# Kernel tuning notes

Measured on AMD Instinct MI355X. Metric: run time of the kernel, lower is better.

The kernel has to match this reference:

```python
import jax, jax.numpy as jnp
import numpy as np
from jax import lax

KH = KW = 3
STRIDE = (1, 1)
PAD = (1, 1)

def setup_inputs() -> dict:
    key = jax.random.key(0)
    k1, k2, k3 = jax.random.split(key, 3)
    B_, C, H, W = 16, 128, 56, 56
    O, R = 256, 16
    Kflat = C * KH * KW
    x = jax.random.normal(k1, (B_, C, H, W), dtype=jnp.float32)
    # kaiming_normal_ fan_out for A: std = sqrt(2/out_channels)
    A = jax.random.normal(k2, (O, R), dtype=jnp.float32) * np.float32(np.sqrt(2.0 / O))
    # kaiming_normal_ fan_in for B: std = sqrt(2/kernel_flat_dim)
    Bm = jax.random.normal(k3, (R, Kflat), dtype=jnp.float32) * np.float32(np.sqrt(2.0 / Kflat))
    return {"x": x, "A": A, "B": Bm}

def reference(x, A, B):
    b, c, h, w = x.shape
    h_out = (h + 2 * PAD[0] - KH) // STRIDE[0] + 1
    w_out = (w + 2 * PAD[1] - KW) // STRIDE[1] + 1
    # im2col: [B, C*KH*KW, H_out, W_out]; feature order (c, kh, kw) matches torch Unfold
    patches = lax.conv_general_dilated_patches(
        x, filter_shape=(KH, KW), window_strides=STRIDE,
        padding=((PAD[0], PAD[0]), (PAD[1], PAD[1])))
    patches = patches.reshape(b, c * KH * KW, h_out * w_out)  # [B, K, L]
    tmp = jnp.einsum('rk,bkl->brl', B, patches)               # rank-limited matmul
    out = jnp.einsum('or,brl->bol', A, tmp)                   # [B, O, L]
    return out.reshape(b, A.shape[0], h_out, w_out)
```

## Files before the change

kernel.cpp:

```cpp
#include <hip/hip_runtime.h>
#include <hip/hip_bf16.h>


#define Bn 16
#define Cc 128
#define Hh 56
#define Ww 56
#define Ll (Hh * Ww)
#define Rr 16
#define Oo 256
#define KF (Cc * 9)
#define NKS 36
#define W2 58
#define RPITCH 128
#define ROWB (W2 * RPITCH)
#define HB 2

typedef __attribute__((ext_vector_type(8))) short bfrag_t;
typedef __attribute__((ext_vector_type(4))) float f32x4;

__device__ __forceinline__ float bf16_bits(unsigned short u) {
    return __uint_as_float(((unsigned)u) << 16);
}

__device__ __forceinline__ unsigned short bf16_rne(float f) {
    const unsigned u = __float_as_uint(f);
    const unsigned r = u + 0x7FFFu + ((u >> 16) & 1u);
    return (unsigned short)(r >> 16);
}

__device__ __forceinline__ bool detect_bf16(const void* __restrict__ p) {
    const unsigned* w = (const unsigned*)p;
    int c = 0;
#pragma unroll
    for (int i = 0; i < 32; ++i) {
        const unsigned e = (w[i] >> 7) & 0xFFu;
        c += (e >= 96u && e <= 144u) ? 1 : 0;
    }
    return c >= 20;
}

__global__ __launch_bounds__(256) void prep_frag(
    const void* __restrict__ A, const void* __restrict__ Bm,
    unsigned short* __restrict__ Bfrag, float* __restrict__ Afp)
{
    const bool ab = detect_bf16(A);
    const bool bb = detect_bf16(Bm);
    const int i = blockIdx.x * 256 + threadIdx.x;
    if (i < NKS * 512) {
        const int kstep = i >> 9, rem = i & 511;
        const int l = rem >> 3, e = rem & 7;
        const int r = l & 15, g = l >> 4;
        const int kp = kstep * 32 + g * 8 + e;
        const int tap = kp >> 7, c = kp & 127;
        const int k = c * 9 + tap;
        const float v = bb ? bf16_bits(((const unsigned short*)Bm)[r * KF + k])
                           : ((const float*)Bm)[r * KF + k];
        const unsigned short hi = bf16_rne(v);
        const float lov = v - bf16_bits(hi);
        Bfrag[(kstep * 2 + 0) * 512 + rem] = hi;
        Bfrag[(kstep * 2 + 1) * 512 + rem] = bf16_rne(lov);
    }
    if (i < Oo * Rr) {
        Afp[i] = ab ? bf16_bits(((const unsigned short*)A)[i])
                    : ((const float*)A)[i];
    }
}

#define MFB(A, B, C) __builtin_amdgcn_mfma_f32_16x16x32_bf16((A), (B), (C), 0, 0, 0)

template<bool XB, bool BB>
__device__ __forceinline__ void fused_body(
    const void* __restrict__ x,
    const unsigned short* __restrict__ Bfrag,
    const float* __restrict__ Afp,
    float* __restrict__ out,
    unsigned short* __restrict__ xs)
{
    const int tid  = threadIdx.x;
    const int lane = tid & 63;
    const int wv   = __builtin_amdgcn_readfirstlane(tid >> 6);
    const int t    = wv & 3;
    const int kh   = wv >> 2;
    const int h0   = blockIdx.x * HB;
    const int b    = blockIdx.y;

    {
        const int l   = lane;
        const bool lok = (l < Ww);
#pragma unroll
        for (int rr = 0; rr < HB + 2; ++rr) {
            const int hh = h0 - 1 + rr;
            unsigned short* xr = xs + rr * ROWB;
            if (hh >= 0 && hh < Hh) {
                if (lok) {
                    const unsigned gb = (unsigned)(b * Cc * Ll + hh * Ww + l);
#pragma unroll
                    for (int it = 0; it < 2; ++it) {
                        const int cs_ = it * 8 + wv;
                        const int c0  = cs_ * 8;
                        bfrag_t v;
#pragma unroll
                        for (int j = 0; j < 8; ++j) {
                            if constexpr (XB) {
                                v[j] = (short)((const unsigned short*)x)[
                                    gb + (unsigned)((c0 + j) * Ll)];
                            } else {
                                v[j] = (short)bf16_rne(((const float*)x)[
                                    gb + (unsigned)((c0 + j) * Ll)]);
                            }
                        }
                        const int sp = cs_ ^ ((l + 1) & 7);
                        *(bfrag_t*)((char*)xr + (l + 1) * 256 + sp * 16) = v;
                    }
                }
            } else {
                unsigned* xw = (unsigned*)xr;
#pragma unroll
                for (int it = 0; it < 7; ++it) xw[it * 512 + tid] = 0u;
                if (tid < 3712 - 7 * 512) xw[7 * 512 + tid] = 0u;
            }
        }
        if (tid < 128) {
#pragma unroll
            for (int rr = 0; rr < HB + 2; ++rr) {
                xs[rr * ROWB + tid] = 0;
                xs[rr * ROWB + 57 * RPITCH + tid] = 0;
            }
        }
    }
    __syncthreads();

    const int col = lane & 15;
    const int g   = lane >> 4;
    const int px  = t * 16 + col;
    const int pxc = px < Ww ? px : Ww - 1;

    unsigned off6[6];
#pragma unroll
    for (int dwv = 0; dwv < 3; ++dwv)
#pragma unroll
        for (int cbi = 0; cbi < 2; ++cbi) {
            const int cb = kh * 2 + cbi;
            const int p2 = pxc + dwv;
            off6[dwv * 2 + cbi] = (unsigned)(p2 * 256 +
                (((cb * 4 + g) ^ (p2 & 7)) << 4));
        }

    f32x4 acc0 = {0.f, 0.f, 0.f, 0.f};
    f32x4 acc1 = {0.f, 0.f, 0.f, 0.f};
    const bfrag_t* __restrict__ bfp = (const bfrag_t*)Bfrag;

#pragma unroll
    for (int tap = 0; tap < 9; ++tap) {
        const int dh = tap / 3, dw = tap - dh * 3;
#pragma unroll
        for (int cbi = 0; cbi < 2; ++cbi) {
            const int cb = kh * 2 + cbi;
            const int ks = tap * 4 + cb;
            const bfrag_t ahi = bfp[(ks * 2 + 0) * 64 + lane];
            const char* p0 = (const char*)xs + dh * (ROWB * 2) + off6[dw * 2 + cbi];
            const bfrag_t pf0 = *(const bfrag_t*)p0;
            const bfrag_t pf1 = *(const bfrag_t*)(p0 + ROWB * 2);
            acc0 = MFB(ahi, pf0, acc0);
            acc1 = MFB(ahi, pf1, acc1);
            if constexpr (!BB) {
                const bfrag_t alo = bfp[(ks * 2 + 1) * 64 + lane];
                acc0 = MFB(alo, pf0, acc0);
                acc1 = MFB(alo, pf1, acc1);
            }
        }
    }

    __syncthreads();
    float (*tmp2)[HB][Rr][66] = (float (*)[HB][Rr][66])xs;

#pragma unroll
    for (int reg = 0; reg < 4; ++reg) {
        tmp2[kh][0][g * 4 + reg][t * 16 + col] = acc0[reg];
        tmp2[kh][1][g * 4 + reg][t * 16 + col] = acc1[reg];
    }
    __syncthreads();

    float tv0[Rr], tv1[Rr];
#pragma unroll
    for (int r = 0; r < Rr; ++r) {
        tv0[r] = tmp2[0][0][r][lane] + tmp2[1][0][r][lane];
        tv1[r] = tmp2[0][1][r][lane] + tmp2[1][1][r][lane];
    }

    const bool wok = (lane < Ww);
    const size_t obase = (size_t)b * Oo * Ll + (size_t)(h0 * Ww) + (size_t)lane;
#pragma unroll 4
    for (int j = 0; j < 32; ++j) {
        const int o = wv * 32 + j;
        const float* Ao = Afp + (size_t)o * Rr;
        float s0 = 0.f, s1 = 0.f;
#pragma unroll
        for (int r = 0; r < Rr; ++r) {
            const float av = Ao[r];
            s0 += av * tv0[r];
            s1 += av * tv1[r];
        }
        if (wok) {
            out[obase + (size_t)o * Ll]      = s0;
            out[obase + (size_t)o * Ll + Ww] = s1;
        }
    }
}

__global__ __launch_bounds__(512, 4) void fused_ks(
    const void* __restrict__ x,
    const void* __restrict__ Bm,
    const unsigned short* __restrict__ Bfrag,
    const float* __restrict__ Afp,
    float* __restrict__ out)
{
    __shared__ __align__(16) unsigned short xs[4 * ROWB];
    const bool xb = detect_bf16(x);
    const bool bb = detect_bf16(Bm);
    if (xb) { if (bb) fused_body<true , true >(x, Bfrag, Afp, out, xs);
              else    fused_body<true , false>(x, Bfrag, Afp, out, xs); }
    else    { if (bb) fused_body<false, true >(x, Bfrag, Afp, out, xs);
              else    fused_body<false, false>(x, Bfrag, Afp, out, xs); }
}

__global__ __launch_bounds__(256) void fused_fallback(
    const void* __restrict__ x, const void* __restrict__ A,
    const void* __restrict__ Bm, float* __restrict__ out)
{
    const bool xb = detect_bf16(x);
    const bool ab = detect_bf16(A);
    const bool bb = detect_bf16(Bm);
    const int gid = blockIdx.x * 256 + threadIdx.x;
    const int b = gid / Ll;
    const int l = gid - b * Ll;
    const int h = l / Ww, w = l - h * Ww;
    float acc[Rr];
#pragma unroll
    for (int r = 0; r < Rr; ++r) acc[r] = 0.f;
    const size_t xbase = (size_t)b * Cc * Ll;
    for (int c = 0; c < Cc; ++c) {
        const size_t xc = xbase + (size_t)c * Ll;
        float xv[9];
#pragma unroll
        for (int dh = 0; dh < 3; ++dh) {
            const int hh = h + dh - 1;
            const bool hok = (hh >= 0) & (hh < Hh);
#pragma unroll
            for (int dw = 0; dw < 3; ++dw) {
                const int ww = w + dw - 1;
                const bool ok = hok & (ww >= 0) & (ww < Ww);
                const size_t idx = xc + (size_t)(hh * Ww + ww);
                xv[dh*3+dw] = ok ? (xb ? bf16_bits(((const unsigned short*)x)[idx])
                                       : ((const float*)x)[idx]) : 0.f;
            }
        }
#pragma unroll
        for (int r = 0; r < Rr; ++r) {
            const size_t bo = (size_t)r * KF + (size_t)c * 9;
            float s = acc[r];
#pragma unroll
            for (int i = 0; i < 9; ++i)
                s += (bb ? bf16_bits(((const unsigned short*)Bm)[bo+i])
                         : ((const float*)Bm)[bo+i]) * xv[i];
            acc[r] = s;
        }
    }
    const size_t obase = (size_t)b * Oo * Ll + (size_t)l;
    for (int o = 0; o < Oo; ++o) {
        float s = 0.f;
#pragma unroll
        for (int r = 0; r < Rr; ++r)
            s += (ab ? bf16_bits(((const unsigned short*)A)[o*Rr+r])
                     : ((const float*)A)[o*Rr+r]) * acc[r];
        out[obase + (size_t)o * Ll] = s;
    }
}

extern "C" void kernel_launch(void* const* d_in, const int* in_sizes, int n_in,
                              void* d_out, int out_size, void* d_ws, size_t ws_size,
                              hipStream_t stream) {
    const void* x  = d_in[0];
    const void* A  = d_in[1];
    const void* Bm = d_in[2];
    for (int i = 0; i < n_in && i < 3; ++i) {
        const int s = in_sizes[i];
        if      (s == Bn * Cc * Ll) x  = d_in[i];
        else if (s == Oo * Rr)      A  = d_in[i];
        else if (s == Rr * KF)      Bm = d_in[i];
    }
    float* out = (float*)d_out;

    const size_t frag_bytes = (size_t)(NKS * 2 * 512) * 2;
    const size_t afp_bytes  = (size_t)(Oo * Rr) * 4;
    const size_t need       = frag_bytes + afp_bytes;

    if (ws_size >= need) {
        unsigned short* Bfrag = (unsigned short*)d_ws;
        float* Afp = (float*)((char*)d_ws + frag_bytes);
        prep_frag<<<dim3(72), 256, 0, stream>>>(A, Bm, Bfrag, Afp);
        fused_ks<<<dim3(Hh / HB, Bn), 512, 0, stream>>>(x, Bm, Bfrag, Afp, out);
    } else {
        fused_fallback<<<dim3((Bn * Ll) / 256), 256, 0, stream>>>(x, A, Bm, out);
    }
}
```

Before: 103.6 us.

## Double block size to 16 waves, splitting channel reduction four ways

```diff
diff --git a/kernel.cpp b/kernel.cpp
--- a/kernel.cpp
+++ b/kernel.cpp
@@ -81,13 +81,15 @@
     const int lane = tid & 63;
     const int wv   = __builtin_amdgcn_readfirstlane(tid >> 6);
     const int t    = wv & 3;
-    const int kh   = wv >> 2;
+    const int kq   = wv >> 2;
     const int h0   = blockIdx.x * HB;
     const int b    = blockIdx.y;
 
     {
         const int l   = lane;
         const bool lok = (l < Ww);
+        const int cs_ = wv;
+        const int c0  = cs_ * 8;
 #pragma unroll
         for (int rr = 0; rr < HB + 2; ++rr) {
             const int hh = h0 - 1 + rr;
@@ -95,30 +97,25 @@
             if (hh >= 0 && hh < Hh) {
                 if (lok) {
                     const unsigned gb = (unsigned)(b * Cc * Ll + hh * Ww + l);
-#pragma unroll
-                    for (int it = 0; it < 2; ++it) {
-                        const int cs_ = it * 8 + wv;
-                        const int c0  = cs_ * 8;
-                        bfrag_t v;
-#pragma unroll
-                        for (int j = 0; j < 8; ++j) {
-                            if constexpr (XB) {
-                                v[j] = (short)((const unsigned short*)x)[
-                                    gb + (unsigned)((c0 + j) * Ll)];
-                            } else {
-                                v[j] = (short)bf16_rne(((const float*)x)[
-                                    gb + (unsigned)((c0 + j) * Ll)]);
-                            }
+                    bfrag_t v;
+#pragma unroll
+                    for (int j = 0; j < 8; ++j) {
+                        if constexpr (XB) {
+                            v[j] = (short)((const unsigned short*)x)[
+                                gb + (unsigned)((c0 + j) * Ll)];
+                        } else {
+                            v[j] = (short)bf16_rne(((const float*)x)[
+                                gb + (unsigned)((c0 + j) * Ll)]);
                         }
-                        const int sp = cs_ ^ ((l + 1) & 7);
-                        *(bfrag_t*)((char*)xr + (l + 1) * 256 + sp * 16) = v;
                     }
+                    const int sp = cs_ ^ ((l + 1) & 7);
+                    *(bfrag_t*)((char*)xr + (l + 1) * 256 + sp * 16) = v;
                 }
             } else {
                 unsigned* xw = (unsigned*)xr;
 #pragma unroll
-                for (int it = 0; it < 7; ++it) xw[it * 512 + tid] = 0u;
-                if (tid < 3712 - 7 * 512) xw[7 * 512 + tid] = 0u;
+                for (int it = 0; it < 3; ++it) xw[it * 1024 + tid] = 0u;
+                if (tid < 3712 - 3 * 1024) xw[3 * 1024 + tid] = 0u;
             }
         }
         if (tid < 128) {
@@ -136,16 +133,12 @@
     const int px  = t * 16 + col;
     const int pxc = px < Ww ? px : Ww - 1;
 
-    unsigned off6[6];
-#pragma unroll
-    for (int dwv = 0; dwv < 3; ++dwv)
-#pragma unroll
-        for (int cbi = 0; cbi < 2; ++cbi) {
-            const int cb = kh * 2 + cbi;
-            const int p2 = pxc + dwv;
-            off6[dwv * 2 + cbi] = (unsigned)(p2 * 256 +
-                (((cb * 4 + g) ^ (p2 & 7)) << 4));
-        }
+    unsigned off3[3];
+#pragma unroll
+    for (int dwv = 0; dwv < 3; ++dwv) {
+        const int p2 = pxc + dwv;
+        off3[dwv] = (unsigned)(p2 * 256 + (((kq * 4 + g) ^ (p2 & 7)) << 4));
+    }
 
     f32x4 acc0 = {0.f, 0.f, 0.f, 0.f};
     f32x4 acc1 = {0.f, 0.f, 0.f, 0.f};
@@ -154,21 +147,17 @@
 #pragma unroll
     for (int tap = 0; tap < 9; ++tap) {
         const int dh = tap / 3, dw = tap - dh * 3;
-#pragma unroll
-        for (int cbi = 0; cbi < 2; ++cbi) {
-            const int cb = kh * 2 + cbi;
-            const int ks = tap * 4 + cb;
-            const bfrag_t ahi = bfp[(ks * 2 + 0) * 64 + lane];
-            const char* p0 = (const char*)xs + dh * (ROWB * 2) + off6[dw * 2 + cbi];
-            const bfrag_t pf0 = *(const bfrag_t*)p0;
-            const bfrag_t pf1 = *(const bfrag_t*)(p0 + ROWB * 2);
-            acc0 = MFB(ahi, pf0, acc0);
-            acc1 = MFB(ahi, pf1, acc1);
-            if constexpr (!BB) {
-                const bfrag_t alo = bfp[(ks * 2 + 1) * 64 + lane];
-                acc0 = MFB(alo, pf0, acc0);
-                acc1 = MFB(alo, pf1, acc1);
-            }
+        const int ks = tap * 4 + kq;
+        const bfrag_t ahi = bfp[(ks * 2 + 0) * 64 + lane];
+        const char* p0 = (const char*)xs + dh * (ROWB * 2) + off3[dw];
+        const bfrag_t pf0 = *(const bfrag_t*)p0;
+        const bfrag_t pf1 = *(const bfrag_t*)(p0 + ROWB * 2);
+        acc0 = MFB(ahi, pf0, acc0);
+        acc1 = MFB(ahi, pf1, acc1);
+        if constexpr (!BB) {
+            const bfrag_t alo = bfp[(ks * 2 + 1) * 64 + lane];
+            acc0 = MFB(alo, pf0, acc0);
+            acc1 = MFB(alo, pf1, acc1);
         }
     }
 
@@ -177,23 +166,25 @@
 
 #pragma unroll
     for (int reg = 0; reg < 4; ++reg) {
-        tmp2[kh][0][g * 4 + reg][t * 16 + col] = acc0[reg];
-        tmp2[kh][1][g * 4 + reg][t * 16 + col] = acc1[reg];
+        tmp2[kq][0][g * 4 + reg][t * 16 + col] = acc0[reg];
+        tmp2[kq][1][g * 4 + reg][t * 16 + col] = acc1[reg];
     }
     __syncthreads();
 
     float tv0[Rr], tv1[Rr];
 #pragma unroll
     for (int r = 0; r < Rr; ++r) {
-        tv0[r] = tmp2[0][0][r][lane] + tmp2[1][0][r][lane];
-        tv1[r] = tmp2[0][1][r][lane] + tmp2[1][1][r][lane];
+        tv0[r] = (tmp2[0][0][r][lane] + tmp2[1][0][r][lane])
+               + (tmp2[2][0][r][lane] + tmp2[3][0][r][lane]);
+        tv1[r] = (tmp2[0][1][r][lane] + tmp2[1][1][r][lane])
+               + (tmp2[2][1][r][lane] + tmp2[3][1][r][lane]);
     }
 
     const bool wok = (lane < Ww);
     const size_t obase = (size_t)b * Oo * Ll + (size_t)(h0 * Ww) + (size_t)lane;
 #pragma unroll 4
-    for (int j = 0; j < 32; ++j) {
-        const int o = wv * 32 + j;
+    for (int j = 0; j < 16; ++j) {
+        const int o = wv * 16 + j;
         const float* Ao = Afp + (size_t)o * Rr;
         float s0 = 0.f, s1 = 0.f;
 #pragma unroll
@@ -209,7 +200,7 @@
     }
 }
 
-__global__ __launch_bounds__(512, 4) void fused_ks(
+__global__ __launch_bounds__(1024, 8) void fused_ks(
     const void* __restrict__ x,
     const void* __restrict__ Bm,
     const unsigned short* __restrict__ Bfrag,
@@ -300,7 +291,7 @@
         unsigned short* Bfrag = (unsigned short*)d_ws;
         float* Afp = (float*)((char*)d_ws + frag_bytes);
         prep_frag<<<dim3(72), 256, 0, stream>>>(A, Bm, Bfrag, Afp);
-        fused_ks<<<dim3(Hh / HB, Bn), 512, 0, stream>>>(x, Bm, Bfrag, Afp, out);
+        fused_ks<<<dim3(Hh / HB, Bn), 1024, 0, stream>>>(x, Bm, Bfrag, Afp, out);
     } else {
         fused_fallback<<<dim3((Bn * Ll) / 256), 256, 0, stream>>>(x, A, Bm, out);
     }
```

Measured after the change: 105.9 us. +2.3%, slower.

## Split fused kernel into rank-projection and output-expansion kernels with XCD-aware mapping

Applied to the files above, without the earlier changes.

```diff
diff --git a/kernel.cpp b/kernel.cpp
--- a/kernel.cpp
+++ b/kernel.cpp
@@ -70,11 +70,10 @@
 #define MFB(A, B, C) __builtin_amdgcn_mfma_f32_16x16x32_bf16((A), (B), (C), 0, 0, 0)
 
 template<bool XB, bool BB>
-__device__ __forceinline__ void fused_body(
+__device__ __forceinline__ void k1_body(
     const void* __restrict__ x,
     const unsigned short* __restrict__ Bfrag,
-    const float* __restrict__ Afp,
-    float* __restrict__ out,
+    float* __restrict__ tmpo,
     unsigned short* __restrict__ xs)
 {
     const int tid  = threadIdx.x;
@@ -82,8 +81,14 @@
     const int wv   = __builtin_amdgcn_readfirstlane(tid >> 6);
     const int t    = wv & 3;
     const int kh   = wv >> 2;
-    const int h0   = blockIdx.x * HB;
-    const int b    = blockIdx.y;
+
+    const int lin  = blockIdx.x;
+    const int xcd  = lin & 7;
+    const int j    = lin >> 3;
+    const int boff = (j >= 28) ? 1 : 0;
+    const int hb   = j - 28 * boff;
+    const int b    = xcd * 2 + boff;
+    const int h0   = hb * HB;
 
     {
         const int l   = lane;
@@ -101,13 +106,13 @@
                         const int c0  = cs_ * 8;
                         bfrag_t v;
 #pragma unroll
-                        for (int j = 0; j < 8; ++j) {
+                        for (int jj = 0; jj < 8; ++jj) {
                             if constexpr (XB) {
-                                v[j] = (short)((const unsigned short*)x)[
-                                    gb + (unsigned)((c0 + j) * Ll)];
+                                v[jj] = (short)((const unsigned short*)x)[
+                                    gb + (unsigned)((c0 + jj) * Ll)];
                             } else {
-                                v[j] = (short)bf16_rne(((const float*)x)[
-                                    gb + (unsigned)((c0 + j) * Ll)]);
+                                v[jj] = (short)bf16_rne(((const float*)x)[
+                                    gb + (unsigned)((c0 + jj) * Ll)]);
                             }
                         }
                         const int sp = cs_ ^ ((l + 1) & 7);
@@ -182,47 +187,62 @@
     }
     __syncthreads();
 
-    float tv0[Rr], tv1[Rr];
-#pragma unroll
-    for (int r = 0; r < Rr; ++r) {
-        tv0[r] = tmp2[0][0][r][lane] + tmp2[1][0][r][lane];
-        tv1[r] = tmp2[0][1][r][lane] + tmp2[1][1][r][lane];
-    }
-
-    const bool wok = (lane < Ww);
-    const size_t obase = (size_t)b * Oo * Ll + (size_t)(h0 * Ww) + (size_t)lane;
-#pragma unroll 4
-    for (int j = 0; j < 32; ++j) {
-        const int o = wv * 32 + j;
-        const float* Ao = Afp + (size_t)o * Rr;
-        float s0 = 0.f, s1 = 0.f;
-#pragma unroll
-        for (int r = 0; r < Rr; ++r) {
-            const float av = Ao[r];
-            s0 += av * tv0[r];
-            s1 += av * tv1[r];
-        }
-        if (wok) {
-            out[obase + (size_t)o * Ll]      = s0;
-            out[obase + (size_t)o * Ll + Ww] = s1;
-        }
-    }
-}
-
-__global__ __launch_bounds__(512, 4) void fused_ks(
+    {
+        const int row  = wv >> 2;
+        const int rgrp = (wv & 3) * 4;
+        if (lane < Ww) {
+#pragma unroll
+            for (int rr = 0; rr < 4; ++rr) {
+                const int r = rgrp + rr;
+                const float v = tmp2[0][row][r][lane] + tmp2[1][row][r][lane];
+                tmpo[(size_t)(b * Rr + r) * Ll + (size_t)((h0 + row) * Ww) + lane] = v;
+            }
+        }
+    }
+}
+
+__global__ __launch_bounds__(512, 4) void k1_tmp(
     const void* __restrict__ x,
     const void* __restrict__ Bm,
     const unsigned short* __restrict__ Bfrag,
-    const float* __restrict__ Afp,
-    float* __restrict__ out)
+    float* __restrict__ tmpo)
 {
     __shared__ __align__(16) unsigned short xs[4 * ROWB];
     const bool xb = detect_bf16(x);
     const bool bb = detect_bf16(Bm);
-    if (xb) { if (bb) fused_body<true , true >(x, Bfrag, Afp, out, xs);
-              else    fused_body<true , false>(x, Bfrag, Afp, out, xs); }
-    else    { if (bb) fused_body<false, true >(x, Bfrag, Afp, out, xs);
-              else    fused_body<false, false>(x, Bfrag, Afp, out, xs); }
+    if (xb) { if (bb) k1_body<true , true >(x, Bfrag, tmpo, xs);
+              else    k1_body<true , false>(x, Bfrag, tmpo, xs); }
+    else    { if (bb) k1_body<false, true >(x, Bfrag, tmpo, xs);
+              else    k1_body<false, false>(x, Bfrag, tmpo, xs); }
+}
+
+__global__ __launch_bounds__(448) void k2_expand(
+    const float* __restrict__ tmp,
+    const float* __restrict__ Afp,
+    float* __restrict__ out)
+{
+    const int gid   = blockIdx.x;
+    const int chunk = gid % 7;
+    const int oc    = (gid / 7) & 7;
+    const int b     = gid / 56;
+    const int l     = chunk * 448 + threadIdx.x;
+
+    const float* tb = tmp + (size_t)(b * Rr) * Ll + l;
+    float t[Rr];
+#pragma unroll
+    for (int r = 0; r < Rr; ++r) t[r] = tb[(size_t)r * Ll];
+
+    const size_t obase = (size_t)(b * Oo) * Ll + (size_t)l;
+    const int o0 = oc * 32;
+#pragma unroll 4
+    for (int j = 0; j < 32; ++j) {
+        const int o = o0 + j;
+        const float* Ao = Afp + (size_t)o * Rr;
+        float s = 0.f;
+#pragma unroll
+        for (int r = 0; r < Rr; ++r) s += Ao[r] * t[r];
+        __builtin_nontemporal_store(s, &out[obase + (size_t)o * Ll]);
+    }
 }
 
 __global__ __launch_bounds__(256) void fused_fallback(
@@ -294,13 +314,16 @@
 
     const size_t frag_bytes = (size_t)(NKS * 2 * 512) * 2;
     const size_t afp_bytes  = (size_t)(Oo * Rr) * 4;
-    const size_t need       = frag_bytes + afp_bytes;
+    const size_t tmp_bytes  = (size_t)Bn * Rr * Ll * 4;
+    const size_t need       = frag_bytes + afp_bytes + tmp_bytes;
 
     if (ws_size >= need) {
         unsigned short* Bfrag = (unsigned short*)d_ws;
-        float* Afp = (float*)((char*)d_ws + frag_bytes);
+        float* Afp  = (float*)((char*)d_ws + frag_bytes);
+        float* tmpo = (float*)((char*)d_ws + frag_bytes + afp_bytes);
         prep_frag<<<dim3(72), 256, 0, stream>>>(A, Bm, Bfrag, Afp);
-        fused_ks<<<dim3(Hh / HB, Bn), 512, 0, stream>>>(x, Bm, Bfrag, Afp, out);
+        k1_tmp   <<<dim3(448), 512, 0, stream>>>(x, Bm, Bfrag, tmpo);
+        k2_expand<<<dim3(896), 448, 0, stream>>>(tmpo, Afp, out);
     } else {
         fused_fallback<<<dim3((Bn * Ll) / 256), 256, 0, stream>>>(x, A, Bm, out);
     }
```

Result: slower. 106.4 us (+2.8%).
